# Kernel optimization log

Measured on AMD Instinct MI355X. Metric: run time of the kernel, lower is better.

Reference implementation:

```python
import jax, jax.numpy as jnp
import numpy as np

NUM_CLASSES = 101
BATCH = 262144
LAMBDA = 1000.0


def setup_inputs() -> dict:
    key = jax.random.key(0)
    k1, k2 = jax.random.split(key)
    outputs = jax.random.normal(k1, (BATCH, NUM_CLASSES), dtype=jnp.float32)
    targets = jax.random.randint(k2, (BATCH,), 0, NUM_CLASSES, dtype=jnp.int64)
    return {"outputs": outputs, "targets": targets}


def reference(outputs, targets):
    B, C = outputs.shape
    targets = targets.reshape(-1)
    tf = targets.astype(outputs.dtype)

    probs = jax.nn.softmax(outputs, axis=1)                      # [B, C]
    labels = jnp.arange(C, dtype=outputs.dtype)                  # [C]
    pred_values = jnp.sum(probs * labels[None, :], axis=1)       # [B]
    centered = labels[None, :] - pred_values[:, None]            # [B, C]
    variance = jnp.sum(probs * centered * centered, axis=1)      # [B]
    variance = jnp.clip(variance, 1e-6, None)
    est_err = (pred_values - tf) ** 2
    concentrated_loss = jnp.mean(0.5 * jnp.log(variance) + est_err / (2.0 * variance))

    # Unimodal ordinal penalty, vectorized over the original double loop:
    # sign_j = -1 if j < target else +1; penalty = relu(-(p_j - p_{j+1}) * sign_j)
    j = jnp.arange(C - 1)                                        # [C-1]
    sign = jnp.where(j[None, :] < targets[:, None], -1.0, 1.0).astype(outputs.dtype)
    prob_diff = probs[:, :-1] - probs[:, 1:]                     # [B, C-1]
    penalty = jax.nn.relu(-prob_diff * sign)
    unimodal_loss = jnp.sum(penalty) / B
    weighted_unimodal_loss = LAMBDA * unimodal_loss

    total_loss = concentrated_loss + weighted_unimodal_loss
    return (total_loss, concentrated_loss, weighted_unimodal_loss)
```

## Files before the change

kernel.cpp:

```cpp
#include <hip/hip_runtime.h>


#define NC 101
#define LAMBDA_W 1000.0

__global__ __launch_bounds__(256)
void ucl_stream_kernel(const float* __restrict__ x,
                       const int* __restrict__ tgt,
                       float2* __restrict__ partial,
                       int ngroups)
{
    const int tid  = threadIdx.x;
    const int lane = tid & 63;
    const int s    = lane & 15;
    const int gwave  = blockIdx.x * 4 + (tid >> 6);
    const int nwaves = gridDim.x * 4;

    float conc = 0.f, pens = 0.f;

    for (int g = gwave; g < ngroups; g += nwaves) {
        const int row = g * 4 + (lane >> 4);
        const float* __restrict__ xr = x + (size_t)row * NC;
        const int t = tgt[row];

        float e[7];
#pragma unroll
        for (int k = 0; k < 7; ++k) {
            const int j = s + 16 * k;
            e[k] = (j < NC) ? xr[j] : 0.f;
        }
#pragma unroll
        for (int k = 0; k < 7; ++k) {
            const int j = s + 16 * k;
            float ee = __expf(e[k]);
            e[k] = (j < NC) ? ee : 0.f;
        }

        float S = 0.f, W = 0.f, Q = 0.f;
#pragma unroll
        for (int k = 0; k < 7; ++k) {
            const float fj = (float)(s + 16 * k);
            S += e[k];
            W = fmaf(e[k], fj, W);
            Q = fmaf(e[k], fj * fj, Q);
        }

        float pen = 0.f;
#pragma unroll
        for (int k = 0; k < 7; ++k) {
            float n1 = __shfl_down(e[k], 1);
            float nx = (k < 6) ? __shfl(e[k + 1], lane & 48)
                               : 0.f;
            float en = (s == 15) ? nx : n1;
            float d  = e[k] - en;
            pen += fmaxf(d, 0.f);
            const int j = s + 16 * k;
            pen -= (j == t) ? e[k] : 0.f;
        }

#pragma unroll
        for (int off = 1; off < 16; off <<= 1) {
            S   += __shfl_xor(S, off);
            W   += __shfl_xor(W, off);
            Q   += __shfl_xor(Q, off);
            pen += __shfl_xor(pen, off);
        }

        if (s == 0) {
            float pred = W / S;
            float var  = fmaxf(fmaf(-pred, pred, Q / S), 1e-6f);
            float err  = pred - (float)t;
            conc += 0.5f * __logf(var) + err * err / (2.0f * var);
            pens += pen / S;
        }
    }

    conc += __shfl_down(conc, 16);
    pens += __shfl_down(pens, 16);
    conc += __shfl_down(conc, 32);
    pens += __shfl_down(pens, 32);

    __shared__ float red[8];
    if (lane == 0) {
        red[(tid >> 6) * 2 + 0] = conc;
        red[(tid >> 6) * 2 + 1] = pens;
    }
    __syncthreads();
    if (tid == 0)
        partial[blockIdx.x] = make_float2(red[0] + red[2] + red[4] + red[6],
                                          red[1] + red[3] + red[5] + red[7]);
}

__global__ __launch_bounds__(256)
void ucl_finalize(const float2* __restrict__ partial,
                  float* __restrict__ out,
                  int nblocks, double invB)
{
    const int tid = threadIdx.x;
    double c = 0.0, p = 0.0;
    for (int i = tid; i < nblocks; i += 256) {
        float2 v = partial[i];
        c += (double)v.x;
        p += (double)v.y;
    }
#pragma unroll
    for (int off = 32; off > 0; off >>= 1) {
        c += __shfl_down(c, off);
        p += __shfl_down(p, off);
    }
    __shared__ double sm[8];
    if ((tid & 63) == 0) { sm[(tid >> 6) * 2] = c; sm[(tid >> 6) * 2 + 1] = p; }
    __syncthreads();
    if (tid == 0) {
        double C = (sm[0] + sm[2] + sm[4] + sm[6]) * invB;
        double P = (sm[1] + sm[3] + sm[5] + sm[7]) * invB * LAMBDA_W;
        out[0] = (float)(C + P);
        out[1] = (float)C;
        out[2] = (float)P;
    }
}

extern "C" void kernel_launch(void* const* d_in, const int* in_sizes, int n_in,
                              void* d_out, int out_size, void* d_ws, size_t ws_size,
                              hipStream_t stream)
{
    const float* x   = (const float*)d_in[0];
    const int*   tgt = (const int*)d_in[1];
    float* out = (float*)d_out;
    float2* partial = (float2*)d_ws;

    const int B = in_sizes[1];
    const int ngroups = B / 4;
    const int blocks = 1024;

    hipLaunchKernelGGL(ucl_stream_kernel, dim3(blocks), dim3(256), 0, stream,
                       x, tgt, partial, ngroups);
    hipLaunchKernelGGL(ucl_finalize, dim3(1), dim3(256), 0, stream,
                       partial, out, blocks, 1.0 / (double)B);
}
```

Measured before the change: 153.9 us.

## Give each lane contiguous row elements, vector loads, and DPP team reductions

```diff
diff --git a/kernel.cpp b/kernel.cpp
--- a/kernel.cpp
+++ b/kernel.cpp
@@ -3,6 +3,25 @@
 
 #define NC 101
 #define LAMBDA_W 1000.0
+
+typedef float f4a __attribute__((ext_vector_type(4), aligned(4)));
+
+__device__ __forceinline__ float team_sum16(float v) {
+    v += __int_as_float(__builtin_amdgcn_update_dpp(
+        0, __float_as_int(v), 0x111, 0xf, 0xf, true));
+    v += __int_as_float(__builtin_amdgcn_update_dpp(
+        0, __float_as_int(v), 0x112, 0xf, 0xf, true));
+    v += __int_as_float(__builtin_amdgcn_update_dpp(
+        0, __float_as_int(v), 0x114, 0xf, 0xf, true));
+    v += __int_as_float(__builtin_amdgcn_update_dpp(
+        0, __float_as_int(v), 0x118, 0xf, 0xf, true));
+    return v;
+}
+
+__device__ __forceinline__ float team_next(float v) {
+    return __int_as_float(__builtin_amdgcn_update_dpp(
+        0, __float_as_int(v), 0x101, 0xf, 0xf, true));
+}
 
 __global__ __launch_bounds__(256)
 void ucl_stream_kernel(const float* __restrict__ x,
@@ -16,57 +35,63 @@
     const int gwave  = blockIdx.x * 4 + (tid >> 6);
     const int nwaves = gridDim.x * 4;
 
+    const int jbase = 8 * s;
+    float fj[8];
+#pragma unroll
+    for (int i = 0; i < 8; ++i) fj[i] = (float)(jbase + i);
+
     float conc = 0.f, pens = 0.f;
 
-    for (int g = gwave; g < ngroups; g += nwaves) {
+    const int per = ngroups / nwaves;
+    const int rem = ngroups - per * nwaves;
+    const int cnt  = per + (gwave < rem ? 1 : 0);
+    const int base = gwave * per + (gwave < rem ? gwave : rem);
+
+    for (int it = 0; it < cnt; ++it) {
+        const int g   = base + it;
         const int row = g * 4 + (lane >> 4);
         const float* __restrict__ xr = x + (size_t)row * NC;
         const int t = tgt[row];
 
-        float e[7];
+        f4a va = {0.f, 0.f, 0.f, 0.f};
+        f4a vb = {0.f, 0.f, 0.f, 0.f};
+        if (s < 13) va = *(const f4a*)(xr + jbase);
+        if (s < 12) vb = *(const f4a*)(xr + jbase + 4);
+        else if (s == 12) vb.x = xr[100];
+
+        float e[8];
 #pragma unroll
-        for (int k = 0; k < 7; ++k) {
-            const int j = s + 16 * k;
-            e[k] = (j < NC) ? xr[j] : 0.f;
-        }
-#pragma unroll
-        for (int k = 0; k < 7; ++k) {
-            const int j = s + 16 * k;
-            float ee = __expf(e[k]);
-            e[k] = (j < NC) ? ee : 0.f;
+        for (int i = 0; i < 4; ++i) {
+            float ea = __expf(va[i]);
+            float eb = __expf(vb[i]);
+            e[i]     = (s < 13) ? ea : 0.f;
+            e[4 + i] = (s < (i == 0 ? 13 : 12)) ? eb : 0.f;
         }
 
         float S = 0.f, W = 0.f, Q = 0.f;
 #pragma unroll
-        for (int k = 0; k < 7; ++k) {
-            const float fj = (float)(s + 16 * k);
-            S += e[k];
-            W = fmaf(e[k], fj, W);
-            Q = fmaf(e[k], fj * fj, Q);
+        for (int i = 0; i < 8; ++i) {
+            float p = e[i] * fj[i];
+            S += e[i];
+            W += p;
+            Q  = fmaf(p, fj[i], Q);
         }
 
+        const float en = team_next(e[0]);
         float pen = 0.f;
 #pragma unroll
-        for (int k = 0; k < 7; ++k) {
-            float n1 = __shfl_down(e[k], 1);
-            float nx = (k < 6) ? __shfl(e[k + 1], lane & 48)
-                               : 0.f;
-            float en = (s == 15) ? nx : n1;
-            float d  = e[k] - en;
-            pen += fmaxf(d, 0.f);
-            const int j = s + 16 * k;
-            pen -= (j == t) ? e[k] : 0.f;
+        for (int i = 0; i < 8; ++i) {
+            float nx = (i < 7) ? e[i + 1] : en;
+            pen += fmaxf(e[i] - nx, 0.f);
+            pen -= (jbase + i == t) ? e[i] : 0.f;
         }
 
-#pragma unroll
-        for (int off = 1; off < 16; off <<= 1) {
-            S   += __shfl_xor(S, off);
-            W   += __shfl_xor(W, off);
-            Q   += __shfl_xor(Q, off);
-            pen += __shfl_xor(pen, off);
-        }
+        S   = team_sum16(S);
+        W   = team_sum16(W);
+        Q   = team_sum16(Q);
+        pen = team_sum16(pen);
 
-        if (s == 0) {
+        if (s == 15) {
             float pred = W / S;
             float var  = fmaxf(fmaf(-pred, pred, Q / S), 1e-6f);
             float err  = pred - (float)t;
@@ -81,7 +106,7 @@
     pens += __shfl_down(pens, 32);
 
     __shared__ float red[8];
-    if (lane == 0) {
+    if (lane == 15) {
         red[(tid >> 6) * 2 + 0] = conc;
         red[(tid >> 6) * 2 + 1] = pens;
     }
@@ -131,7 +156,7 @@
 
     const int B = in_sizes[1];
     const int ngroups = B / 4;
-    const int blocks = 1024;
+    const int blocks = 2048;
 
     hipLaunchKernelGGL(ucl_stream_kernel, dim3(blocks), dim3(256), 0, stream,
                        x, tgt, partial, ngroups);
```

New measurement: 161.3 us. 4.8% more time.
